# Optimization experiments

Measured on AMD Instinct MI355X. Metric: run time of the kernel, lower is better.

The kernel has to match this reference:

```python
import jax, jax.numpy as jnp
import numpy as np
from jax.scipy.special import logsumexp

S, B, T = 512, 1024, 48


def setup_inputs() -> dict:
    key = jax.random.key(0)
    k1, k2, k3, k4, k5 = jax.random.split(key, 5)
    return {
        "emissions": jax.random.normal(k1, (S, B, T), jnp.float32),
        "tags": jax.random.randint(k2, (S, B), 0, T, jnp.int32),
        "mask": jnp.ones((S, B), jnp.float32),
        "transitions": jax.random.normal(k3, (T, T), jnp.float32),
        "start_transitions": jax.random.normal(k4, (T,), jnp.float32),
        "stop_transitions": jax.random.normal(k5, (T,), jnp.float32),
    }


def _crf(emissions, tags, mask, transitions, start, stop):
    # emissions: (S,B,T), tags/mask: (S,B), time-major as in the torch module
    init = start[None, :] + emissions[0]  # (B,T)

    def step(carry, inp):
        fv, vv = carry  # forward (logsumexp) and viterbi (max) vars, each (B,T)
        em, m = inp  # (B,T), (B,)
        # scores[b, next, prev] = prev_var + transitions[prev,next] swapped to match
        # torch: forward_var.unsqueeze(1) + emission.unsqueeze(2) + transitions.unsqueeze(0)
        sc_f = fv[:, None, :] + transitions[None, :, :] + em[:, :, None]  # (B,T,T)
        sc_v = vv[:, None, :] + transitions[None, :, :] + em[:, :, None]
        new_fv = logsumexp(sc_f, axis=2)
        new_vv = jnp.max(sc_v, axis=2)
        m_ = m[:, None]
        fv = m_ * new_fv + (1.0 - m_) * fv
        vv = m_ * new_vv + (1.0 - m_) * vv
        return (fv, vv), None

    (fv, vv), _ = jax.lax.scan(step, (init, init), (emissions[1:], mask[1:]))
    alpha = logsumexp(fv + stop[None, :], axis=1)  # total_score (B,)
    best_path_score = jnp.max(vv + stop[None, :], axis=1)  # (B,)

    # real (gold) path score, fully vectorized over time
    em_tag = jnp.take_along_axis(emissions, tags[:, :, None].astype(jnp.int32), axis=2)[:, :, 0]  # (S,B)
    trans_sc = transitions[tags[:-1], tags[1:]]  # (S-1,B)
    real = (start[tags[0]]
            + jnp.sum(mask[1:] * (trans_sc + em_tag[1:]), axis=0)
            + stop[tags[-1]])
    loss = jnp.mean(alpha - real)
    return loss, real, alpha, best_path_score


def reference(emissions, tags, mask, transitions, start_transitions, stop_transitions):
    # Training-mode forward (return_best_path=False -> best_path is None in torch)
    return _crf(emissions, tags, mask, transitions, start_transitions, stop_transitions)
```

## Files before the change

### kernel.cpp

```cpp
#include <hip/hip_runtime.h>
#include <hip/hip_fp16.h>

#define S_LEN 512
#define B_DIM 1024
#define T_DIM 48
#define L2E 1.4426950408889634f
#define LN2 0.6931471805599453f

#define EXP2F(x) __builtin_amdgcn_exp2f(x)
#define LOG2F(x) __builtin_amdgcn_logf(x)

typedef _Float16 h2v __attribute__((ext_vector_type(2)));
typedef _Float16 r4  __attribute__((ext_vector_type(4)));
typedef float    f4  __attribute__((ext_vector_type(4)));

__device__ __forceinline__ f4 MFMA16(r4 a, r4 b, f4 c) {
#if defined(__HIP_DEVICE_COMPILE__)
  return __builtin_amdgcn_mfma_f32_16x16x16f16(a, b, c, 0, 0, 0);
#else
  (void)a; (void)b; return c;
#endif
}

__device__ __forceinline__ __half2 hmax2(__half2 a, __half2 b) {
  h2v r = __builtin_elementwise_max(__builtin_bit_cast(h2v, a),
                                    __builtin_bit_cast(h2v, b));
  return __builtin_bit_cast(__half2, r);
}
__device__ __forceinline__ __half2 bpick(__half2 src, int lane) {
  int s = __builtin_amdgcn_readlane(__builtin_bit_cast(int, src), lane);
  return __builtin_bit_cast(__half2, s);
}

template <int CTRL, int RMASK>
__device__ __forceinline__ float dppmovf(float v) {
  return __int_as_float(__builtin_amdgcn_update_dpp(
      __float_as_int(v), __float_as_int(v), CTRL, RMASK, 0xF, false));
}
template <int CTRL, int RMASK>
__device__ __forceinline__ float dppmaxf(float m) {
  return fmaxf(m, dppmovf<CTRL, RMASK>(m));
}
template <int CTRL, int RMASK>
__device__ __forceinline__ float dppaddf(float m) {
  return m + dppmovf<CTRL, RMASK>(m);
}
__device__ __forceinline__ float wave_max63(float m) {
  m = dppmaxf<0xB1, 0xF>(m);  m = dppmaxf<0x4E, 0xF>(m);
  m = dppmaxf<0x141, 0xF>(m); m = dppmaxf<0x140, 0xF>(m);
  m = dppmaxf<0x142, 0xA>(m); m = dppmaxf<0x143, 0xC>(m);
  return __int_as_float(__builtin_amdgcn_readlane(__float_as_int(m), 63));
}
__device__ __forceinline__ float wave_sum63(float m) {
  m = dppaddf<0xB1, 0xF>(m);  m = dppaddf<0x4E, 0xF>(m);
  m = dppaddf<0x141, 0xF>(m); m = dppaddf<0x140, 0xF>(m);
  m = dppaddf<0x142, 0xA>(m); m = dppaddf<0x143, 0xC>(m);
  return __int_as_float(__builtin_amdgcn_readlane(__float_as_int(m), 63));
}

__global__ __launch_bounds__(128, 2)
void crf_fused(const float* __restrict__ em, const int* __restrict__ tags,
               const float* __restrict__ mask, const float* __restrict__ trans,
               const float* __restrict__ startT, const float* __restrict__ stopT,
               float* __restrict__ out)
{
  const int blk  = blockIdx.x;
  const int wave = threadIdx.x >> 6;
  const int l    = threadIdx.x & 63;

  if (blk >= B_DIM) {
    const int tile = (blk - B_DIM) * 2 + wave;
    const int a  = l >> 4;
    const int n  = l & 15;
    const int bb = tile * 16 + n;
    const int bpi = (l ^ 32) << 2;

#define DECL_A(mt,kf) r4 A##mt##kf; {                                  \
      const float* tb = trans + (16*(mt) + n) * T_DIM + 16*(kf) + 4*a; \
      A##mt##kf[0] = (_Float16)EXP2F(tb[0] * L2E);                     \
      A##mt##kf[1] = (_Float16)EXP2F(tb[1] * L2E);                     \
      A##mt##kf[2] = (_Float16)EXP2F(tb[2] * L2E);                     \
      A##mt##kf[3] = (_Float16)EXP2F(tb[3] * L2E); }
    DECL_A(0,0) DECL_A(0,1) DECL_A(0,2)
    DECL_A(1,0) DECL_A(1,1) DECL_A(1,2)
    DECL_A(2,0) DECL_A(2,1) DECL_A(2,2)
    asm volatile("" : "+v"(A00), "+v"(A01), "+v"(A02),
                      "+v"(A10), "+v"(A11), "+v"(A12),
                      "+v"(A20), "+v"(A21), "+v"(A22));

    const float* e0 = em + (size_t)bb * T_DIM;
    f4 P0, P1, P2;
#pragma unroll
    for (int r = 0; r < 4; ++r) {
      P0[r] = EXP2F((startT[ 0 + 4*a + r] + e0[ 0 + 4*a + r]) * L2E);
      P1[r] = EXP2F((startT[16 + 4*a + r] + e0[16 + 4*a + r]) * L2E);
      P2[r] = EXP2F((startT[32 + 4*a + r] + e0[32 + 4*a + r]) * L2E);
    }
    float k2 = 0.f;

    float mx0 = fmaxf(fmaxf(fmaxf(P0[0],P0[1]), fmaxf(P0[2],P0[3])),
               fmaxf(fmaxf(fmaxf(P1[0],P1[1]), fmaxf(P1[2],P1[3])),
                     fmaxf(fmaxf(P2[0],P2[1]), fmaxf(P2[2],P2[3]))));
    mx0 = fmaxf(mx0, __int_as_float(__builtin_amdgcn_ds_swizzle(
                       __float_as_int(mx0), 0x401F)));
    mx0 = fmaxf(mx0, __int_as_float(__builtin_amdgcn_ds_bpermute(
                       bpi, __float_as_int(mx0))));
    int ee0 = (__float_as_int(mx0) >> 23) - 126;
    int eeA = ee0, eeB = ee0;

    const size_t rstep = (size_t)B_DIM * T_DIM;
    const float* pe = em + rstep + (size_t)bb * T_DIM + 4*a;
    f4 EA0 = *(const f4*)(pe +  0), EA1 = *(const f4*)(pe + 16),
       EA2 = *(const f4*)(pe + 32);
    pe += rstep;
    f4 EB0 = *(const f4*)(pe +  0), EB1 = *(const f4*)(pe + 16),
       EB2 = *(const f4*)(pe + 32);
    pe += rstep;
    f4 EC0 = *(const f4*)(pe +  0), EC1 = *(const f4*)(pe + 16),
       EC2 = *(const f4*)(pe + 32);
    pe += rstep;
    float mkA = mask[1*B_DIM + bb], mkB = mask[2*B_DIM + bb],
          mkC = mask[3*B_DIM + bb];
    const float* pm = mask + 4*B_DIM + bb;

#define FMSTEP(LOAD)                                                      \
    { f4 D0, D1, D2; float mkD;                                           \
      if (LOAD) { D0 = *(const f4*)(pe); D1 = *(const f4*)(pe + 16);      \
                  D2 = *(const f4*)(pe + 32); pe += rstep;                \
                  mkD = *pm; pm += B_DIM; }                               \
      else      { D0 = EC0; D1 = EC1; D2 = EC2; mkD = mkC; }              \
      int eh = eeA >> 1;                       \
      eh = eh > 60 ? 60 : (eh < -60 ? -60 : eh);                          \
      eeA = eeB;                                                          \
      float c = __int_as_float((121 - eh) << 23);          \
      k2 += (float)(eh + 6);                                              \
      r4 B0, B1, B2;                                                      \
      B0[0]=(_Float16)(P0[0]*c); B0[1]=(_Float16)(P0[1]*c);               \
      B0[2]=(_Float16)(P0[2]*c); B0[3]=(_Float16)(P0[3]*c);               \
      B1[0]=(_Float16)(P1[0]*c); B1[1]=(_Float16)(P1[1]*c);               \
      B1[2]=(_Float16)(P1[2]*c); B1[3]=(_Float16)(P1[3]*c);               \
      B2[0]=(_Float16)(P2[0]*c); B2[1]=(_Float16)(P2[1]*c);               \
      B2[2]=(_Float16)(P2[2]*c); B2[3]=(_Float16)(P2[3]*c);               \
      f4 Z = {0.f, 0.f, 0.f, 0.f};                                        \
      f4 C0 = MFMA16(A00, B0, Z); C0 = MFMA16(A01, B1, C0);               \
      C0 = MFMA16(A02, B2, C0);                                           \
      f4 C1 = MFMA16(A10, B0, Z); C1 = MFMA16(A11, B1, C1);               \
      C1 = MFMA16(A12, B2, C1);                                           \
      f4 C2 = MFMA16(A20, B0, Z); C2 = MFMA16(A21, B1, C2);               \
      C2 = MFMA16(A22, B2, C2);                                           \
      _Pragma("unroll")                                                   \
      for (int r = 0; r < 4; ++r) {                                       \
        float ps0 = P0[r]*c, q0 = C0[r]*EXP2F(EA0[r]*L2E);                \
        P0[r] = fmaf(mkA, q0 - ps0, ps0);                                 \
        float ps1 = P1[r]*c, q1 = C1[r]*EXP2F(EA1[r]*L2E);                \
        P1[r] = fmaf(mkA, q1 - ps1, ps1);                                 \
        float ps2 = P2[r]*c, q2 = C2[r]*EXP2F(EA2[r]*L2E);                \
        P2[r] = fmaf(mkA, q2 - ps2, ps2);                                 \
      }                                                                   \
       \
      float mx = fmaxf(fmaxf(fmaxf(P0[0],P0[1]), fmaxf(P0[2],P0[3])),     \
                 fmaxf(fmaxf(fmaxf(P1[0],P1[1]), fmaxf(P1[2],P1[3])),     \
                       fmaxf(fmaxf(P2[0],P2[1]), fmaxf(P2[2],P2[3]))));   \
      mx = fmaxf(mx, __int_as_float(__builtin_amdgcn_ds_swizzle(          \
                       __float_as_int(mx), 0x401F)));                     \
      mx = fmaxf(mx, __int_as_float(__builtin_amdgcn_ds_bpermute(         \
                       bpi, __float_as_int(mx))));                        \
      eeB = (__float_as_int(mx) >> 23) - 126;                             \
      EA0 = EB0; EA1 = EB1; EA2 = EB2;                                    \
      EB0 = EC0; EB1 = EC1; EB2 = EC2;                                    \
      EC0 = D0;  EC1 = D1;  EC2 = D2;                                     \
      mkA = mkB; mkB = mkC; mkC = mkD; }

#pragma unroll 2
    for (int s = 1; s <= 508; ++s) FMSTEP(true)
    FMSTEP(false) FMSTEP(false) FMSTEP(false)

    float part = 0.f;
#pragma unroll
    for (int r = 0; r < 4; ++r) {
      part = fmaf(P0[r], EXP2F(stopT[ 0 + 4*a + r] * L2E), part);
      part = fmaf(P1[r], EXP2F(stopT[16 + 4*a + r] * L2E), part);
      part = fmaf(P2[r], EXP2F(stopT[32 + 4*a + r] * L2E), part);
    }
    part += __int_as_float(__builtin_amdgcn_ds_swizzle(
                __float_as_int(part), 0x401F));
    part += __int_as_float(__builtin_amdgcn_ds_bpermute(
                bpi, __float_as_int(part)));
    float alpha = LN2 * (k2 + LOG2F(part));
    if (a == 0) out[1 + B_DIM + bb] = alpha;
    return;
  }

  if (wave == 1) {
    const int b = blk;
    float acc = 0.f;
#pragma unroll
    for (int k = 0; k < 8; ++k) {
      int s = 1 + l + (k << 6);
      if (s < S_LEN) {
        int   tp  = tags[(s - 1) * B_DIM + b];
        int   tc  = tags[s * B_DIM + b];
        float mkv = mask[s * B_DIM + b];
        float emt = em[((size_t)s * B_DIM + b) * T_DIM + tc];
        acc = fmaf(mkv, trans[tp * T_DIM + tc] + emt, acc);
      }
    }
    float tot = wave_sum63(acc);
    if (l == 0)
      out[1 + b] = startT[tags[b]] +
                   stopT[tags[(S_LEN - 1) * B_DIM + b]] + tot;
    return;
  }

  const int b  = blk;
  const int ri = (l < T_DIM) ? l : (T_DIM - 1);
  const float* emb = em + (size_t)b * T_DIM + ri;
  const size_t estep = (size_t)B_DIM * T_DIM;
  float e1 = emb[1*estep], e2 = emb[2*estep], e3 = emb[3*estep];
  float e4 = emb[4*estep], e5 = emb[5*estep], e6 = emb[6*estep];
  float mk1 = mask[1*B_DIM + b], mk2 = mask[2*B_DIM + b];
  float mk3 = mask[3*B_DIM + b], mk4 = mask[4*B_DIM + b];
  float mk5 = mask[5*B_DIM + b], mk6 = mask[6*B_DIM + b];
  const float* pf  = emb + 7*estep;
  const float* pmk = mask + 7*B_DIM + b;

#define SHIFT_REGS                                                   \
      e1 = e2; e2 = e3; e3 = e4; e4 = e5; e5 = e6; e6 = ep;          \
      mk1 = mk2; mk2 = mk3; mk3 = mk4; mk4 = mk5; mk5 = mk6; mk6 = mkp;

#define DECL_T(nn) __half2 T##nn = __floats2half2_rn( \
      trans[ri * T_DIM + 2*(nn)], trans[ri * T_DIM + 2*(nn) + 1]);
  DECL_T(0)  DECL_T(1)  DECL_T(2)  DECL_T(3)  DECL_T(4)  DECL_T(5)
  DECL_T(6)  DECL_T(7)  DECL_T(8)  DECL_T(9)  DECL_T(10) DECL_T(11)
  DECL_T(12) DECL_T(13) DECL_T(14) DECL_T(15) DECL_T(16) DECL_T(17)
  DECL_T(18) DECL_T(19) DECL_T(20) DECL_T(21) DECL_T(22) DECL_T(23)

  asm volatile("" : "+v"(T0), "+v"(T1), "+v"(T2), "+v"(T3),
    "+v"(T4), "+v"(T5), "+v"(T6), "+v"(T7), "+v"(T8), "+v"(T9),
    "+v"(T10), "+v"(T11), "+v"(T12), "+v"(T13), "+v"(T14),
    "+v"(T15), "+v"(T16), "+v"(T17), "+v"(T18), "+v"(T19),
    "+v"(T20), "+v"(T21), "+v"(T22), "+v"(T23));

  float v = startT[ri] + emb[0];
  const __half2 NEGI = __floats2half2_rn(-60000.f, -60000.f);
  float m_ref = wave_max63(v);

#define VVG(g, Ta, Tb, Tc, Td, Te, Tf)                 \
    { __half2 t0 = bpick(vp, 12*(g) + 0);              \
      __half2 t1 = bpick(vp, 12*(g) + 2);              \
      __half2 t2 = bpick(vp, 12*(g) + 4);              \
      __half2 t3 = bpick(vp, 12*(g) + 6);              \
      __half2 t4 = bpick(vp, 12*(g) + 8);              \
      __half2 t5 = bpick(vp, 12*(g) + 10);             \
      m0 = hmax2(m0, __hadd2(t0, Ta));                 \
      m1 = hmax2(m1, __hadd2(t1, Tb));                 \
      m2 = hmax2(m2, __hadd2(t2, Tc));                 \
      m3 = hmax2(m3, __hadd2(t3, Td));                 \
      m0 = hmax2(m0, __hadd2(t4, Te));                 \
      m1 = hmax2(m1, __hadd2(t5, Tf)); }

#define VV_STEP(LOAD, DOTREE)                                        \
    { float ep, mkp;                                                 \
      if (LOAD) { ep = *pf; pf += estep; mkp = *pmk; pmk += B_DIM; } \
      else      { ep = e6; mkp = mk6; }                              \
      if (DOTREE) m_ref = wave_max63(v);                             \
      float vr  = v - m_ref;                                         \
      float vn_ = dppmovf<0xB1, 0xF>(vr);                            \
      __half2 vp = __floats2half2_rn(vr, vn_);                       \
      __half2 m0 = NEGI, m1 = NEGI, m2 = NEGI, m3 = NEGI;            \
      VVG(0, T0,  T1,  T2,  T3,  T4,  T5)                            \
      VVG(1, T6,  T7,  T8,  T9,  T10, T11)                           \
      VVG(2, T12, T13, T14, T15, T16, T17)                           \
      VVG(3, T18, T19, T20, T21, T22, T23)                           \
      m0 = hmax2(hmax2(m0, m1), hmax2(m2, m3));                      \
      float mx = fmaxf(__low2float(m0), __high2float(m0));           \
      float vnew = e1 + m_ref + mx;                                  \
      v = fmaf(mk1, vnew - v, v);                                    \
      SHIFT_REGS }

#pragma unroll 8
  for (int s = 1; s <= 504; ++s) VV_STEP(true, ((s & 7) == 0))
  VV_STEP(true, false)
  VV_STEP(false, false) VV_STEP(false, false) VV_STEP(false, false)
  VV_STEP(false, false) VV_STEP(false, false) VV_STEP(false, false)

  float best = wave_max63(v + stopT[ri]);
  if (l == 0) out[1 + 2 * B_DIM + b] = best;
}

__global__ __launch_bounds__(256)
void crf_loss(float* __restrict__ out)
{
  __shared__ float red[256];
  int t = threadIdx.x;
  float a = 0.f;
  for (int b = t; b < B_DIM; b += 256)
    a += out[1 + B_DIM + b] - out[1 + b];
  red[t] = a;
  __syncthreads();
  for (int w = 128; w > 0; w >>= 1) {
    if (t < w) red[t] += red[t + w];
    __syncthreads();
  }
  if (t == 0) out[0] = red[0] * (1.0f / B_DIM);
}

extern "C" void kernel_launch(void* const* d_in, const int* in_sizes, int n_in,
                              void* d_out, int out_size, void* d_ws, size_t ws_size,
                              hipStream_t stream) {
  (void)in_sizes; (void)n_in; (void)d_ws; (void)ws_size; (void)out_size;
  const float* em     = (const float*)d_in[0];
  const int*   tags   = (const int*)d_in[1];
  const float* mask   = (const float*)d_in[2];
  const float* trans  = (const float*)d_in[3];
  const float* startT = (const float*)d_in[4];
  const float* stopT  = (const float*)d_in[5];
  float* out = (float*)d_out;

  hipLaunchKernelGGL(crf_fused, dim3(B_DIM + 32), dim3(128), 0, stream,
                     em, tags, mask, trans, startT, stopT, out);
  hipLaunchKernelGGL(crf_loss, dim3(1), dim3(256), 0, stream, out);
}
```

Baseline: 245.2 us.

## Move MFMA forward blocks first and precompute next-step emission exponentials

The 32 MFMA-based forward-algorithm blocks now get the lowest block indices, so they are scheduled first instead of after the 1024 per-batch viterbi/gold blocks. This keeps the long serial chain off the tail of the grid. The emission prefetch pipeline is also deepened by one stage, and the exp2 of the next step's emissions is computed one iteration ahead, taking those exp instructions off the critical MFMA-to-update dependency chain. The cost is more registers for the extra pipeline stage.

```diff
diff --git a/kernel.cpp b/kernel.cpp
--- a/kernel.cpp
+++ b/kernel.cpp
@@ -68,8 +68,8 @@
   const int wave = threadIdx.x >> 6;
   const int l    = threadIdx.x & 63;
 
-  if (blk >= B_DIM) {
-    const int tile = (blk - B_DIM) * 2 + wave;
+  if (blk < 32) {
+    const int tile = blk * 2 + wave;
     const int a  = l >> 4;
     const int n  = l & 15;
     const int bb = tile * 16 + n;
@@ -110,25 +110,37 @@
 
     const size_t rstep = (size_t)B_DIM * T_DIM;
     const float* pe = em + rstep + (size_t)bb * T_DIM + 4*a;
-    f4 EA0 = *(const f4*)(pe +  0), EA1 = *(const f4*)(pe + 16),
-       EA2 = *(const f4*)(pe + 32);
+    f4 XA0, XA1, XA2;
+    {
+      f4 t0 = *(const f4*)(pe), t1 = *(const f4*)(pe + 16),
+         t2 = *(const f4*)(pe + 32);
+#pragma unroll
+      for (int r = 0; r < 4; ++r) {
+        XA0[r] = EXP2F(t0[r] * L2E);
+        XA1[r] = EXP2F(t1[r] * L2E);
+        XA2[r] = EXP2F(t2[r] * L2E);
+      }
+    }
     pe += rstep;
-    f4 EB0 = *(const f4*)(pe +  0), EB1 = *(const f4*)(pe + 16),
+    f4 EB0 = *(const f4*)(pe), EB1 = *(const f4*)(pe + 16),
        EB2 = *(const f4*)(pe + 32);
     pe += rstep;
-    f4 EC0 = *(const f4*)(pe +  0), EC1 = *(const f4*)(pe + 16),
+    f4 EC0 = *(const f4*)(pe), EC1 = *(const f4*)(pe + 16),
        EC2 = *(const f4*)(pe + 32);
     pe += rstep;
+    f4 ED0 = *(const f4*)(pe), ED1 = *(const f4*)(pe + 16),
+       ED2 = *(const f4*)(pe + 32);
+    pe += rstep;
     float mkA = mask[1*B_DIM + bb], mkB = mask[2*B_DIM + bb],
-          mkC = mask[3*B_DIM + bb];
-    const float* pm = mask + 4*B_DIM + bb;
+          mkC = mask[3*B_DIM + bb], mkD = mask[4*B_DIM + bb];
+    const float* pm = mask + 5*B_DIM + bb;
 
 #define FMSTEP(LOAD)                                                      \
-    { f4 D0, D1, D2; float mkD;                                           \
+    { f4 D0, D1, D2; float mkN;                                           \
       if (LOAD) { D0 = *(const f4*)(pe); D1 = *(const f4*)(pe + 16);      \
                   D2 = *(const f4*)(pe + 32); pe += rstep;                \
-                  mkD = *pm; pm += B_DIM; }                               \
-      else      { D0 = EC0; D1 = EC1; D2 = EC2; mkD = mkC; }              \
+                  mkN = *pm; pm += B_DIM; }                               \
+      else      { D0 = ED0; D1 = ED1; D2 = ED2; mkN = mkD; }              \
       int eh = eeA >> 1;                       \
       eh = eh > 60 ? 60 : (eh < -60 ? -60 : eh);                          \
       eeA = eeB;                                                          \
@@ -148,13 +160,21 @@
       C1 = MFMA16(A12, B2, C1);                                           \
       f4 C2 = MFMA16(A20, B0, Z); C2 = MFMA16(A21, B1, C2);               \
       C2 = MFMA16(A22, B2, C2);                                           \
+         \
+      f4 XN0, XN1, XN2;                                                   \
       _Pragma("unroll")                                                   \
       for (int r = 0; r < 4; ++r) {                                       \
-        float ps0 = P0[r]*c, q0 = C0[r]*EXP2F(EA0[r]*L2E);                \
+        XN0[r] = EXP2F(EB0[r] * L2E);                                     \
+        XN1[r] = EXP2F(EB1[r] * L2E);                                     \
+        XN2[r] = EXP2F(EB2[r] * L2E);                                     \
+      }                                                                   \
+      _Pragma("unroll")                                                   \
+      for (int r = 0; r < 4; ++r) {                                       \
+        float ps0 = P0[r]*c, q0 = C0[r]*XA0[r];                           \
         P0[r] = fmaf(mkA, q0 - ps0, ps0);                                 \
-        float ps1 = P1[r]*c, q1 = C1[r]*EXP2F(EA1[r]*L2E);                \
+        float ps1 = P1[r]*c, q1 = C1[r]*XA1[r];                           \
         P1[r] = fmaf(mkA, q1 - ps1, ps1);                                 \
-        float ps2 = P2[r]*c, q2 = C2[r]*EXP2F(EA2[r]*L2E);                \
+        float ps2 = P2[r]*c, q2 = C2[r]*XA2[r];                           \
         P2[r] = fmaf(mkA, q2 - ps2, ps2);                                 \
       }                                                                   \
        \
@@ -166,14 +186,16 @@
       mx = fmaxf(mx, __int_as_float(__builtin_amdgcn_ds_bpermute(         \
                        bpi, __float_as_int(mx))));                        \
       eeB = (__float_as_int(mx) >> 23) - 126;                             \
-      EA0 = EB0; EA1 = EB1; EA2 = EB2;                                    \
+      XA0 = XN0; XA1 = XN1; XA2 = XN2;                                    \
       EB0 = EC0; EB1 = EC1; EB2 = EC2;                                    \
-      EC0 = D0;  EC1 = D1;  EC2 = D2;                                     \
-      mkA = mkB; mkB = mkC; mkC = mkD; }
+      EC0 = ED0; EC1 = ED1; EC2 = ED2;                                    \
+      ED0 = D0;  ED1 = D1;  ED2 = D2;                                     \
+      mkA = mkB; mkB = mkC; mkC = mkD; mkD = mkN; }
 
 #pragma unroll 2
-    for (int s = 1; s <= 508; ++s) FMSTEP(true)
-    FMSTEP(false) FMSTEP(false) FMSTEP(false)
+    for (int s = 1; s <= 507; ++s) FMSTEP(true)
+    FMSTEP(false) FMSTEP(false)
+    FMSTEP(false) FMSTEP(false)
 
     float part = 0.f;
 #pragma unroll
@@ -191,8 +213,9 @@
     return;
   }
 
+  const int b = blk - 32;
+
   if (wave == 1) {
-    const int b = blk;
     float acc = 0.f;
 #pragma unroll
     for (int k = 0; k < 8; ++k) {
@@ -212,7 +235,6 @@
     return;
   }
 
-  const int b  = blk;
   const int ri = (l < T_DIM) ? l : (T_DIM - 1);
   const float* emb = em + (size_t)b * T_DIM + ri;
   const size_t estep = (size_t)B_DIM * T_DIM;
```

New measurement: 230.5 us. 6.0% less time.
